# Optimization experiments

Measured on AMD Instinct MI355X. Metric: run time of the kernel, lower is better.

The kernel has to match this reference:

```python
import jax, jax.numpy as jnp
import numpy as np

N = 50000          # nodes
E = 800000         # edges
IN_C = 128
HID = 64
NUM_GRAPHS = 256
OUT_C = 8


def setup_inputs() -> dict:
    key = jax.random.key(0)
    k1, k2, k3, k4, k5, k6, k7 = jax.random.split(key, 7)
    x = jax.random.normal(k1, (N, IN_C), dtype=jnp.float32)
    edge_index = jax.random.randint(k2, (2, E), 0, N, dtype=jnp.int64)
    batch = jnp.sort(jax.random.randint(k3, (N,), 0, NUM_GRAPHS, dtype=jnp.int64))
    # GCNConv params (lin: in->hid, glorot-ish) and fc params (hid->8)
    W = jax.random.normal(k4, (IN_C, HID), dtype=jnp.float32) / np.sqrt(IN_C)
    b = jnp.zeros((HID,), dtype=jnp.float32)
    Wfc = jax.random.normal(k5, (HID, OUT_C), dtype=jnp.float32) / np.sqrt(HID)
    bfc = jnp.zeros((OUT_C,), dtype=jnp.float32)
    return {"x": x, "edge_index": edge_index, "batch": batch,
            "W": W, "b": b, "Wfc": Wfc, "bfc": bfc}


def reference(x, edge_index, batch, W, b, Wfc, bfc):
    n = x.shape[0]
    # GCNConv: linear transform first, then normalized propagation w/ self-loops
    x_lin = x @ W                                             # [N, HID]
    self_loops = jnp.arange(n, dtype=edge_index.dtype)
    row = jnp.concatenate([edge_index[0], self_loops])        # src
    col = jnp.concatenate([edge_index[1], self_loops])        # dst
    # symmetric normalization: deg over destinations (weight = 1)
    deg = jax.ops.segment_sum(jnp.ones_like(col, dtype=x.dtype), col,
                              num_segments=n)                 # [N]
    dinv = jnp.where(deg > 0, jax.lax.rsqrt(deg), 0.0)
    norm = dinv[row] * dinv[col]                              # [E+N]
    msg = x_lin[row] * norm[:, None]                          # gather + scale
    h = jax.ops.segment_sum(msg, col, num_segments=n) + b     # scatter-add
    h = jax.nn.relu(h)
    # global_mean_pool over batch ids
    sums = jax.ops.segment_sum(h, batch, num_segments=NUM_GRAPHS)
    cnts = jax.ops.segment_sum(jnp.ones((n,), dtype=x.dtype), batch,
                               num_segments=NUM_GRAPHS)
    pooled = sums / jnp.maximum(cnts, 1.0)[:, None]           # [G, HID]
    return pooled @ Wfc + bfc                                 # [G, 8]
```

## Files before the change

### kernel.cpp

```cpp
#include <hip/hip_runtime.h>
#include <stdint.h>

#define N_NODES 50000
#define N_EDGES 800000
#define IN_C    128
#define HID     64
#define NUM_G   256
#define OUT_C   8

#define NBH   64
#define ES    (N_EDGES / NBH)
#define NBIN  50048
#define NPK   (NBIN / 2)

#define NQ_H   4
#define BINS_H (NBIN / NQ_H)
#define PK_H   (BINS_H / 2)
#define NQ_S   8
#define BINS_S (NBIN / NQ_S)

#define NBLK_CSR 98

__device__ __forceinline__ void gload_lds16(const void* g, void* l) {
    __builtin_amdgcn_global_load_lds(
        (const __attribute__((address_space(1))) unsigned int*)g,
        (__attribute__((address_space(3))) unsigned int*)l, 16, 0, 0);
}

__device__ __forceinline__ unsigned short f2bf(float f) {
    union { float f; unsigned u; } v; v.f = f;
    unsigned r = v.u + 0x7fff + ((v.u >> 16) & 1);
    return (unsigned short)(r >> 16);
}

__device__ __forceinline__ float4 bf4(uint2 u) {
    union { unsigned u; float f; } a, b, c, d;
    a.u = u.x << 16;
    b.u = u.x & 0xffff0000u;
    c.u = u.y << 16;
    d.u = u.y & 0xffff0000u;
    return make_float4(a.f, b.f, c.f, d.f);
}

__global__ __launch_bounds__(256) void k_histB(const int* __restrict__ col,
                                               int* __restrict__ part,
                                               int* __restrict__ doneCnt) {
    __shared__ int lh[PK_H];
    const int tid = threadIdx.x;
    if (blockIdx.x == 0 && tid == 0)
        __hip_atomic_store(doneCnt, 0, __ATOMIC_RELAXED, __HIP_MEMORY_SCOPE_AGENT);
    const int r = blockIdx.x >> 2;
    const int q = blockIdx.x & 3;
    const int q0 = q * BINS_H;
    for (int i = tid; i < PK_H; i += 256) lh[i] = 0;
    __syncthreads();
    const int4* col4 = (const int4*)(col + r * ES);
#pragma unroll 2
    for (int j4 = tid; j4 < ES / 4; j4 += 256) {
        int4 c = col4[j4];
        unsigned d0 = (unsigned)(c.x - q0), d1 = (unsigned)(c.y - q0);
        unsigned d2 = (unsigned)(c.z - q0), d3 = (unsigned)(c.w - q0);
        if (d0 < BINS_H) atomicAdd(&lh[d0 >> 1], 1 << ((d0 & 1) * 16));
        if (d1 < BINS_H) atomicAdd(&lh[d1 >> 1], 1 << ((d1 & 1) * 16));
        if (d2 < BINS_H) atomicAdd(&lh[d2 >> 1], 1 << ((d2 & 1) * 16));
        if (d3 < BINS_H) atomicAdd(&lh[d3 >> 1], 1 << ((d3 & 1) * 16));
    }
    __syncthreads();
    int* dst = part + r * NPK + q * PK_H;
    for (int i = tid; i < PK_H; i += 256) dst[i] = lh[i];
}

__global__ __launch_bounds__(256) void k_csr(int* __restrict__ part,
                                             float* __restrict__ dinv,
                                             int* __restrict__ nstart,
                                             const int* __restrict__ batch,
                                             int* __restrict__ gstart,
                                             float* __restrict__ pooled,
                                             int* __restrict__ agg,
                                             int* __restrict__ doneCnt) {
    __shared__ int sScan[256];
    __shared__ int sAgg[NBLK_CSR];
    __shared__ int sPrefix;
    const int tid = threadIdx.x;
    const int b   = blockIdx.x;
    const int t   = b * 256 + tid;
    const bool valid = t < NPK;

    int s0 = 0, s1 = 0;
    if (valid) {
        int idx = t;
#pragma unroll 4
        for (int r = 0; r < NBH; ++r, idx += NPK) {
            int v = part[idx];
            part[idx] = s0 | (s1 << 16);
            s0 += v & 0xffff;
            s1 += (v >> 16) & 0xffff;
        }
        ((float2*)dinv)[t] = make_float2(rsqrtf((float)(s0 + 1)),
                                         rsqrtf((float)(s1 + 1)));
    }

    int ps = s0 + s1;
    sScan[tid] = ps;
    __syncthreads();
    int acc = ps;
#pragma unroll
    for (int off = 1; off < 256; off <<= 1) {
        int tv = (tid >= off) ? sScan[tid - off] : 0;
        __syncthreads();
        acc += tv;
        sScan[tid] = acc;
        __syncthreads();
    }
    const int excl  = acc - ps;
    const int total = sScan[255];

    if (tid == 0) {
        __hip_atomic_store(&agg[b], total, __ATOMIC_RELAXED, __HIP_MEMORY_SCOPE_AGENT);
        __hip_atomic_fetch_add(doneCnt, 1, __ATOMIC_RELEASE, __HIP_MEMORY_SCOPE_AGENT);
        while (__hip_atomic_load(doneCnt, __ATOMIC_ACQUIRE, __HIP_MEMORY_SCOPE_AGENT) < NBLK_CSR)
            __builtin_amdgcn_s_sleep(1);
    }
    __syncthreads();
    if (tid < NBLK_CSR)
        sAgg[tid] = __hip_atomic_load(&agg[tid], __ATOMIC_RELAXED, __HIP_MEMORY_SCOPE_AGENT);
    __syncthreads();
    if (tid == 0) {
        int p = 0;
        for (int j = 0; j < b; ++j) p += sAgg[j];
        sPrefix = p;
    }
    __syncthreads();

    if (valid) {
        int base = sPrefix + excl;
        ((int2*)nstart)[t] = make_int2(base, base + s0);
    }
    if (t <= NUM_G) {
        int lo = 0, hi = N_NODES;
        while (lo < hi) {
            int mid = (lo + hi) >> 1;
            if (batch[mid] < t) lo = mid + 1; else hi = mid;
        }
        gstart[t] = lo;
    }
    if (t < NUM_G * HID) pooled[t] = 0.f;
}

__global__ __launch_bounds__(256) void k_scat2(const int* __restrict__ row,
                                               const int* __restrict__ col,
                                               const int* __restrict__ part,
                                               const int* __restrict__ nstart,
                                               int* __restrict__ ed) {
    __shared__ int lc[BINS_S];
    const int tid = threadIdx.x;
    const int r = blockIdx.x >> 3;
    const int q = blockIdx.x & 7;
    const int q0 = q * BINS_S;
    for (int i = tid; i < BINS_S; i += 256) {
        int bin = q0 + i;
        int bb = part[r * NPK + (bin >> 1)];
        int off = (i & 1) ? ((bb >> 16) & 0xffff) : (bb & 0xffff);
        lc[i] = nstart[bin] + off;
    }
    __syncthreads();
    const int4* col4 = (const int4*)(col + r * ES);
    const int4* row4 = (const int4*)(row + r * ES);
#pragma unroll 2
    for (int j4 = tid; j4 < ES / 4; j4 += 256) {
        int4 c = col4[j4];
        int4 s = row4[j4];
        unsigned d0 = (unsigned)(c.x - q0), d1 = (unsigned)(c.y - q0);
        unsigned d2 = (unsigned)(c.z - q0), d3 = (unsigned)(c.w - q0);
        if (d0 < BINS_S) ed[atomicAdd(&lc[d0], 1)] = s.x;
        if (d1 < BINS_S) ed[atomicAdd(&lc[d1], 1)] = s.y;
        if (d2 < BINS_S) ed[atomicAdd(&lc[d2], 1)] = s.z;
        if (d3 < BINS_S) ed[atomicAdd(&lc[d3], 1)] = s.w;
    }
}

__global__ __launch_bounds__(256) void k_lin(const float* __restrict__ x,
                                             const float* __restrict__ W,
                                             const float* __restrict__ dinv,
                                             unsigned short* __restrict__ yb) {
    __shared__ float xs[64 * IN_C];
    __shared__ float Ws[IN_C * HID];
    const int tid = threadIdx.x;
    const size_t row0 = (size_t)blockIdx.x * 64;
    const int ln = tid & 63, wv = tid >> 6;

    {
        const char* wsrc = (const char*)W;
#pragma unroll
        for (int it = 0; it < 8; ++it) {
            int c = wv * 8 + it;
            gload_lds16(wsrc + c * 1024 + ln * 16, (char*)Ws + c * 1024);
        }
    }
    if (row0 + 64 <= N_NODES) {
        const char* gsrc = (const char*)(x + row0 * IN_C);
#pragma unroll
        for (int it = 0; it < 8; ++it) {
            int c = wv * 8 + it;
            gload_lds16(gsrc + c * 1024 + ln * 16, (char*)xs + c * 1024);
        }
    } else {
        const float4* src = (const float4*)(x + row0 * IN_C);
        for (int i4 = tid; i4 < 2048; i4 += 256) {
            int r = i4 >> 5;
            float4 v = make_float4(0.f, 0.f, 0.f, 0.f);
            if (row0 + r < N_NODES) v = src[i4];
            ((float4*)xs)[i4] = v;
        }
    }
    __syncthreads();

    const int ty = tid >> 4, tx = tid & 15;
    const int r0 = ty * 4, c0 = tx * 4;
    float acc[4][4] = {};

#define AC(ai, kk) ((kk)==0 ? av##ai.x : (kk)==1 ? av##ai.y : (kk)==2 ? av##ai.z : av##ai.w)
#define ROWF(ai, kk, bv) \
    acc[ai][0] = fmaf(AC(ai,kk), bv.x, acc[ai][0]); \
    acc[ai][1] = fmaf(AC(ai,kk), bv.y, acc[ai][1]); \
    acc[ai][2] = fmaf(AC(ai,kk), bv.z, acc[ai][2]); \
    acc[ai][3] = fmaf(AC(ai,kk), bv.w, acc[ai][3]);
#define K4(kk, bv) ROWF(0,kk,bv) ROWF(1,kk,bv) ROWF(2,kk,bv) ROWF(3,kk,bv)

    for (int k = 0; k < IN_C; k += 4) {
        float4 av0 = *(const float4*)&xs[(r0+0)*IN_C + k];
        float4 av1 = *(const float4*)&xs[(r0+1)*IN_C + k];
        float4 av2 = *(const float4*)&xs[(r0+2)*IN_C + k];
        float4 av3 = *(const float4*)&xs[(r0+3)*IN_C + k];
        float4 bv0 = *(const float4*)&Ws[(k+0)*HID + c0];
        float4 bv1 = *(const float4*)&Ws[(k+1)*HID + c0];
        float4 bv2 = *(const float4*)&Ws[(k+2)*HID + c0];
        float4 bv3 = *(const float4*)&Ws[(k+3)*HID + c0];
        K4(0, bv0) K4(1, bv1) K4(2, bv2) K4(3, bv3)
    }
#undef K4
#undef ROWF
#undef AC

#pragma unroll
    for (int i = 0; i < 4; ++i) {
        size_t r = row0 + r0 + i;
        if (r < N_NODES) {
            float dv = dinv[r];
            ushort4 o;
            o.x = f2bf(acc[i][0] * dv);
            o.y = f2bf(acc[i][1] * dv);
            o.z = f2bf(acc[i][2] * dv);
            o.w = f2bf(acc[i][3] * dv);
            *(ushort4*)&yb[r * HID + c0] = o;
        }
    }
}

#define NPT 8
__global__ __launch_bounds__(256) void k_gpool(const int* __restrict__ ed,
                                               const int* __restrict__ nstart,
                                               const float* __restrict__ dinv,
                                               const unsigned short* __restrict__ yb,
                                               const int* __restrict__ batch,
                                               const float* __restrict__ bias,
                                               float* __restrict__ pooled) {
    const int lane = threadIdx.x & 63;
    const int grp  = lane >> 4;
    const int sl   = lane & 15;
    const int node0 = (blockIdx.x * 4 + (threadIdx.x >> 6)) * NPT;
    if (node0 >= N_NODES) return;
    const float4 b4 = *(const float4*)&bias[4 * sl];
    float4 pacc = make_float4(0.f, 0.f, 0.f, 0.f);
    int    cur  = -1;
#pragma unroll 1
    for (int t0 = 0; t0 < NPT; ++t0) {
        int node = node0 + t0;
        if (node >= N_NODES) break;
        const int n0 = nstart[node], n1 = nstart[node + 1];
        float4 facc = make_float4(0.f, 0.f, 0.f, 0.f);
        int t = n0 + grp;
        const int nfull8 = n0 + ((n1 - n0) & ~7);
#pragma unroll 1
        for (; t < nfull8; t += 8) {
            int srcA = ed[t];
            int srcB = ed[t + 4];
            uint2 ua = *(const uint2*)&yb[(size_t)srcA * HID + 4 * sl];
            uint2 ub = *(const uint2*)&yb[(size_t)srcB * HID + 4 * sl];
            float4 va = bf4(ua), vb = bf4(ub);
            facc.x += va.x + vb.x;
            facc.y += va.y + vb.y;
            facc.z += va.z + vb.z;
            facc.w += va.w + vb.w;
        }
#pragma unroll
        for (int step = 0; step < 2; ++step) {
            bool act = t < n1;
            int tt = act ? t : 0;
            int src = ed[tt];
            uint2 u = *(const uint2*)&yb[(size_t)src * HID + 4 * sl];
            if (act) {
                float4 v = bf4(u);
                facc.x += v.x; facc.y += v.y; facc.z += v.z; facc.w += v.w;
            }
            t += 4;
        }
        facc.x += __shfl_xor(facc.x, 16, 64);
        facc.y += __shfl_xor(facc.y, 16, 64);
        facc.z += __shfl_xor(facc.z, 16, 64);
        facc.w += __shfl_xor(facc.w, 16, 64);
        facc.x += __shfl_xor(facc.x, 32, 64);
        facc.y += __shfl_xor(facc.y, 32, 64);
        facc.z += __shfl_xor(facc.z, 32, 64);
        facc.w += __shfl_xor(facc.w, 32, 64);
        uint2 us = *(const uint2*)&yb[(size_t)node * HID + 4 * sl];
        float4 vs = bf4(us);
        float dv = dinv[node];
        float4 hv;
        hv.x = fmaxf((facc.x + vs.x) * dv + b4.x, 0.f);
        hv.y = fmaxf((facc.y + vs.y) * dv + b4.y, 0.f);
        hv.z = fmaxf((facc.z + vs.z) * dv + b4.z, 0.f);
        hv.w = fmaxf((facc.w + vs.w) * dv + b4.w, 0.f);
        int bg = batch[node];
        if (bg != cur) {
            if (cur >= 0 && grp == 0) {
                atomicAdd(&pooled[cur * HID + 4 * sl + 0], pacc.x);
                atomicAdd(&pooled[cur * HID + 4 * sl + 1], pacc.y);
                atomicAdd(&pooled[cur * HID + 4 * sl + 2], pacc.z);
                atomicAdd(&pooled[cur * HID + 4 * sl + 3], pacc.w);
            }
            cur  = bg;
            pacc = hv;
        } else {
            pacc.x += hv.x; pacc.y += hv.y; pacc.z += hv.z; pacc.w += hv.w;
        }
    }
    if (cur >= 0 && grp == 0) {
        atomicAdd(&pooled[cur * HID + 4 * sl + 0], pacc.x);
        atomicAdd(&pooled[cur * HID + 4 * sl + 1], pacc.y);
        atomicAdd(&pooled[cur * HID + 4 * sl + 2], pacc.z);
        atomicAdd(&pooled[cur * HID + 4 * sl + 3], pacc.w);
    }
}

__global__ void k_out(const float* __restrict__ pooled, const int* __restrict__ gstart,
                      const float* __restrict__ Wfc, const float* __restrict__ bfc,
                      float* __restrict__ out) {
    int idx = blockIdx.x * blockDim.x + threadIdx.x;
    int g = idx >> 3;
    int o = idx & 7;
    float inv = 1.f / fmaxf((float)(gstart[g + 1] - gstart[g]), 1.f);
    float acc = 0.f;
#pragma unroll
    for (int k = 0; k < HID; ++k) acc += pooled[g * HID + k] * Wfc[k * OUT_C + o];
    out[idx] = acc * inv + bfc[o];
}

extern "C" void kernel_launch(void* const* d_in, const int* in_sizes, int n_in,
                              void* d_out, int out_size, void* d_ws, size_t ws_size,
                              hipStream_t stream) {
    const float* x     = (const float*)d_in[0];
    const int*   eidx  = (const int*)d_in[1];
    const int*   batch = (const int*)d_in[2];
    const float* W     = (const float*)d_in[3];
    const float* b     = (const float*)d_in[4];
    const float* Wfc   = (const float*)d_in[5];
    const float* bfc   = (const float*)d_in[6];
    float*       out   = (float*)d_out;

    const int* row = eidx;
    const int* col = eidx + N_EDGES;

    char* p = (char*)d_ws;
    int*            part = (int*)p;
    unsigned short* yb   = (unsigned short*)p;
    p += (size_t)NBH * NPK * 4;
    float* dinv   = (float*)p;  p += (size_t)NBIN * 4;
    float* pooled = (float*)p;  p += (size_t)NUM_G * HID * 4;
    int*   nstart = (int*)p;    p += (size_t)(NBIN + 4) * 4;
    int*   gstart = (int*)p;    p += 1040;
    int*   agg    = (int*)p;    p += 400;
    int*   doneCnt= (int*)p;    p += 16;
    int*   ed     = (int*)p;

    k_histB <<<NBH * NQ_H, 256, 0, stream>>>(col, part, doneCnt);
    k_csr   <<<NBLK_CSR, 256, 0, stream>>>(part, dinv, nstart, batch, gstart, pooled, agg, doneCnt);
    k_scat2 <<<NBH * NQ_S, 256, 0, stream>>>(row, col, part, nstart, ed);
    k_lin   <<<(N_NODES + 63) / 64, 256, 0, stream>>>(x, W, dinv, yb);
    k_gpool <<<(N_NODES + 4 * NPT - 1) / (4 * NPT), 256, 0, stream>>>(ed, nstart, dinv, yb, batch, b, pooled);
    k_out   <<<8, 256, 0, stream>>>(pooled, gstart, Wfc, bfc, out);
}
```

Baseline: 102.3 us.

## Fuse CSR build and linear transform into one persistent kernel with packed edges

Merges histogram, scan, and scatter into one kernel using grid-wide spin barriers, and runs the x@W GEMM concurrently in extra blocks of the same launch. Edges are packed as a 16-bit source id plus an fp16 precomputed norm, which removes the dinv scaling from the GEMM epilogue. The final FC layer runs in the last-finishing gpool block instead of a separate launch. This cuts the launch count from six to three and overlaps the GEMM with graph construction. In exchange it depends on all build blocks being co-resident for the spin barriers, and adds fp16 rounding of the norms.

```diff
diff --git a/kernel.cpp b/kernel.cpp
--- a/kernel.cpp
+++ b/kernel.cpp
@@ -1,4 +1,5 @@
 #include <hip/hip_runtime.h>
+#include <hip/hip_fp16.h>
 #include <stdint.h>
 
 #define N_NODES 50000
@@ -16,344 +17,345 @@
 #define NQ_H   4
 #define BINS_H (NBIN / NQ_H)
 #define PK_H   (BINS_H / 2)
-#define NQ_S   8
+#define NQ_S   4
 #define BINS_S (NBIN / NQ_S)
 
-#define NBLK_CSR 98
-
-__device__ __forceinline__ void gload_lds16(const void* g, void* l) {
-    __builtin_amdgcn_global_load_lds(
-        (const __attribute__((address_space(1))) unsigned int*)g,
-        (__attribute__((address_space(3))) unsigned int*)l, 16, 0, 0);
-}
+#define NBLK_CSR   98
+#define NBLK_BUILD 256
+#define NBLK_LIN   512
+#define NTILE      1563
+#define GPOOL_GRID 1563
 
 __device__ __forceinline__ unsigned short f2bf(float f) {
     union { float f; unsigned u; } v; v.f = f;
     unsigned r = v.u + 0x7fff + ((v.u >> 16) & 1);
     return (unsigned short)(r >> 16);
 }
-
 __device__ __forceinline__ float4 bf4(uint2 u) {
     union { unsigned u; float f; } a, b, c, d;
-    a.u = u.x << 16;
-    b.u = u.x & 0xffff0000u;
-    c.u = u.y << 16;
-    d.u = u.y & 0xffff0000u;
+    a.u = u.x << 16;  b.u = u.x & 0xffff0000u;
+    c.u = u.y << 16;  d.u = u.y & 0xffff0000u;
     return make_float4(a.f, b.f, c.f, d.f);
 }
-
-__global__ __launch_bounds__(256) void k_histB(const int* __restrict__ col,
-                                               int* __restrict__ part,
-                                               int* __restrict__ doneCnt) {
-    __shared__ int lh[PK_H];
-    const int tid = threadIdx.x;
-    if (blockIdx.x == 0 && tid == 0)
-        __hip_atomic_store(doneCnt, 0, __ATOMIC_RELAXED, __HIP_MEMORY_SCOPE_AGENT);
-    const int r = blockIdx.x >> 2;
-    const int q = blockIdx.x & 3;
-    const int q0 = q * BINS_H;
-    for (int i = tid; i < PK_H; i += 256) lh[i] = 0;
-    __syncthreads();
-    const int4* col4 = (const int4*)(col + r * ES);
-#pragma unroll 2
-    for (int j4 = tid; j4 < ES / 4; j4 += 256) {
-        int4 c = col4[j4];
-        unsigned d0 = (unsigned)(c.x - q0), d1 = (unsigned)(c.y - q0);
-        unsigned d2 = (unsigned)(c.z - q0), d3 = (unsigned)(c.w - q0);
-        if (d0 < BINS_H) atomicAdd(&lh[d0 >> 1], 1 << ((d0 & 1) * 16));
-        if (d1 < BINS_H) atomicAdd(&lh[d1 >> 1], 1 << ((d1 & 1) * 16));
-        if (d2 < BINS_H) atomicAdd(&lh[d2 >> 1], 1 << ((d2 & 1) * 16));
-        if (d3 < BINS_H) atomicAdd(&lh[d3 >> 1], 1 << ((d3 & 1) * 16));
-    }
-    __syncthreads();
-    int* dst = part + r * NPK + q * PK_H;
-    for (int i = tid; i < PK_H; i += 256) dst[i] = lh[i];
-}
-
-__global__ __launch_bounds__(256) void k_csr(int* __restrict__ part,
-                                             float* __restrict__ dinv,
-                                             int* __restrict__ nstart,
-                                             const int* __restrict__ batch,
-                                             int* __restrict__ gstart,
-                                             float* __restrict__ pooled,
-                                             int* __restrict__ agg,
-                                             int* __restrict__ doneCnt) {
-    __shared__ int sScan[256];
-    __shared__ int sAgg[NBLK_CSR];
-    __shared__ int sPrefix;
+__device__ __forceinline__ float h2f(unsigned hu) {
+    union { __half h; unsigned short u; } c; c.u = (unsigned short)hu;
+    return __half2float(c.h);
+}
+
+__global__ void k_z(float* __restrict__ pooled, int* __restrict__ cnt) {
+    int i = blockIdx.x * 256 + threadIdx.x;
+    pooled[i] = 0.f;
+    if (i < 8) cnt[i] = 0;
+}
+
+__global__ __launch_bounds__(256, 3) void k_build(
+        const int* __restrict__ row, const int* __restrict__ col,
+        const int* __restrict__ batch,
+        const float* __restrict__ x, const float* __restrict__ W,
+        int* __restrict__ part, float* __restrict__ dinv,
+        int* __restrict__ nstart, int* __restrict__ gstart,
+        unsigned* __restrict__ ed, unsigned short* __restrict__ yb,
+        int* __restrict__ agg, int* __restrict__ cnt) {
+    __shared__ int smemI[12512];
     const int tid = threadIdx.x;
     const int b   = blockIdx.x;
-    const int t   = b * 256 + tid;
-    const bool valid = t < NPK;
-
-    int s0 = 0, s1 = 0;
-    if (valid) {
-        int idx = t;
+
+    if (b >= NBLK_BUILD) {
+        float* xs = (float*)smemI;
+        float* Ws = (float*)smemI + 4224;
+        {
+            const float4* wsrc = (const float4*)W;
+            float4*       wdst = (float4*)Ws;
+#pragma unroll
+            for (int j = 0; j < 8; ++j) wdst[tid + 256 * j] = wsrc[tid + 256 * j];
+        }
+        const int ty = tid >> 4, tx = tid & 15;
+        const int r0 = ty * 2, c0 = tx * 4;
+        for (int tile = b - NBLK_BUILD; tile < NTILE; tile += NBLK_LIN) {
+            const int row0 = tile * 32;
+            __syncthreads();
+            {
+                const float4* src = (const float4*)(x + (size_t)row0 * IN_C);
+                for (int i4 = tid; i4 < 1024; i4 += 256) {
+                    int r = i4 >> 5, c4 = i4 & 31;
+                    float4 v = make_float4(0.f, 0.f, 0.f, 0.f);
+                    if (row0 + r < N_NODES) v = src[i4];
+                    *(float4*)&xs[r * 132 + c4 * 4] = v;
+                }
+            }
+            __syncthreads();
+            float acc[2][4] = {};
+#define FMA4(a_, bv_, r_) { acc[r_][0]=fmaf(a_,bv_.x,acc[r_][0]); acc[r_][1]=fmaf(a_,bv_.y,acc[r_][1]); \
+                            acc[r_][2]=fmaf(a_,bv_.z,acc[r_][2]); acc[r_][3]=fmaf(a_,bv_.w,acc[r_][3]); }
+            for (int k = 0; k < IN_C; k += 4) {
+                float4 a0 = *(float4*)&xs[(r0 + 0) * 132 + k];
+                float4 a1 = *(float4*)&xs[(r0 + 1) * 132 + k];
+                float4 b0 = *(const float4*)&Ws[(k + 0) * HID + c0];
+                float4 b1 = *(const float4*)&Ws[(k + 1) * HID + c0];
+                float4 b2 = *(const float4*)&Ws[(k + 2) * HID + c0];
+                float4 b3 = *(const float4*)&Ws[(k + 3) * HID + c0];
+                FMA4(a0.x, b0, 0) FMA4(a0.y, b1, 0) FMA4(a0.z, b2, 0) FMA4(a0.w, b3, 0)
+                FMA4(a1.x, b0, 1) FMA4(a1.y, b1, 1) FMA4(a1.z, b2, 1) FMA4(a1.w, b3, 1)
+            }
+#undef FMA4
+#pragma unroll
+            for (int i = 0; i < 2; ++i) {
+                int r = row0 + r0 + i;
+                if (r < N_NODES) {
+                    ushort4 o;
+                    o.x = f2bf(acc[i][0]); o.y = f2bf(acc[i][1]);
+                    o.z = f2bf(acc[i][2]); o.w = f2bf(acc[i][3]);
+                    *(ushort4*)&yb[(size_t)r * HID + c0] = o;
+                }
+            }
+        }
+        return;
+    }
+
+    {
+        int* lh = smemI;
+        const int rr = b >> 2, q = b & 3, q0 = q * BINS_H;
+        for (int i = tid; i < PK_H; i += 256) lh[i] = 0;
+        __syncthreads();
+        const int4* col4 = (const int4*)(col + rr * ES);
+        for (int j4 = tid; j4 < ES / 4; j4 += 256) {
+            int4 c = col4[j4];
+            unsigned d0 = (unsigned)(c.x - q0), d1 = (unsigned)(c.y - q0);
+            unsigned d2 = (unsigned)(c.z - q0), d3 = (unsigned)(c.w - q0);
+            if (d0 < BINS_H) atomicAdd(&lh[d0 >> 1], 1 << ((d0 & 1) * 16));
+            if (d1 < BINS_H) atomicAdd(&lh[d1 >> 1], 1 << ((d1 & 1) * 16));
+            if (d2 < BINS_H) atomicAdd(&lh[d2 >> 1], 1 << ((d2 & 1) * 16));
+            if (d3 < BINS_H) atomicAdd(&lh[d3 >> 1], 1 << ((d3 & 1) * 16));
+        }
+        __syncthreads();
+        int* dst = part + rr * NPK + q * PK_H;
+        for (int i = tid; i < PK_H; i += 256) dst[i] = lh[i];
+        __syncthreads();
+    }
+    if (tid == 0) {
+        __hip_atomic_fetch_add(&cnt[0], 1, __ATOMIC_RELEASE, __HIP_MEMORY_SCOPE_AGENT);
+        while (__hip_atomic_load(&cnt[0], __ATOMIC_ACQUIRE, __HIP_MEMORY_SCOPE_AGENT) < NBLK_BUILD)
+            __builtin_amdgcn_s_sleep(2);
+    }
+    __syncthreads();
+
+    if (b < NBLK_CSR) {
+        int* sScan   = smemI;
+        int* sAgg    = smemI + 256;
+        int* sPrefix = smemI + 256 + 128;
+        const int t = b * 256 + tid;
+        const bool valid = t < NPK;
+        int s0 = 0, s1 = 0;
+        if (valid) {
+            int idx = t;
 #pragma unroll 4
-        for (int r = 0; r < NBH; ++r, idx += NPK) {
-            int v = part[idx];
-            part[idx] = s0 | (s1 << 16);
-            s0 += v & 0xffff;
-            s1 += (v >> 16) & 0xffff;
-        }
-        ((float2*)dinv)[t] = make_float2(rsqrtf((float)(s0 + 1)),
-                                         rsqrtf((float)(s1 + 1)));
-    }
-
-    int ps = s0 + s1;
-    sScan[tid] = ps;
+            for (int r = 0; r < NBH; ++r, idx += NPK) {
+                int v = part[idx];
+                part[idx] = s0 | (s1 << 16);
+                s0 += v & 0xffff;
+                s1 += (v >> 16) & 0xffff;
+            }
+            ((float2*)dinv)[t] = make_float2(rsqrtf((float)(s0 + 1)),
+                                             rsqrtf((float)(s1 + 1)));
+        }
+        int ps = s0 + s1;
+        sScan[tid] = ps;
+        __syncthreads();
+        int acc = ps;
+#pragma unroll
+        for (int off = 1; off < 256; off <<= 1) {
+            int tv = (tid >= off) ? sScan[tid - off] : 0;
+            __syncthreads();
+            acc += tv;
+            sScan[tid] = acc;
+            __syncthreads();
+        }
+        const int excl  = acc - ps;
+        const int total = sScan[255];
+        if (tid == 0) {
+            __hip_atomic_store(&agg[b], total, __ATOMIC_RELAXED, __HIP_MEMORY_SCOPE_AGENT);
+            __hip_atomic_fetch_add(&cnt[1], 1, __ATOMIC_RELEASE, __HIP_MEMORY_SCOPE_AGENT);
+            while (__hip_atomic_load(&cnt[1], __ATOMIC_ACQUIRE, __HIP_MEMORY_SCOPE_AGENT) < NBLK_CSR)
+                __builtin_amdgcn_s_sleep(2);
+        }
+        __syncthreads();
+        if (tid < NBLK_CSR)
+            sAgg[tid] = __hip_atomic_load(&agg[tid], __ATOMIC_RELAXED, __HIP_MEMORY_SCOPE_AGENT);
+        __syncthreads();
+        if (tid == 0) {
+            int p = 0;
+            for (int j = 0; j < b; ++j) p += sAgg[j];
+            sPrefix[0] = p;
+        }
+        __syncthreads();
+        if (valid) {
+            int base = sPrefix[0] + excl;
+            ((int2*)nstart)[t] = make_int2(base, base + s0);
+        }
+        if (t <= NUM_G) {
+            int lo = 0, hi = N_NODES;
+            while (lo < hi) {
+                int mid = (lo + hi) >> 1;
+                if (batch[mid] < t) lo = mid + 1; else hi = mid;
+            }
+            gstart[t] = lo;
+        }
+        __syncthreads();
+        if (tid == 0)
+            __hip_atomic_fetch_add(&cnt[2], 1, __ATOMIC_RELEASE, __HIP_MEMORY_SCOPE_AGENT);
+    }
+    if (tid == 0) {
+        while (__hip_atomic_load(&cnt[2], __ATOMIC_ACQUIRE, __HIP_MEMORY_SCOPE_AGENT) < NBLK_CSR)
+            __builtin_amdgcn_s_sleep(2);
+    }
     __syncthreads();
-    int acc = ps;
-#pragma unroll
-    for (int off = 1; off < 256; off <<= 1) {
-        int tv = (tid >= off) ? sScan[tid - off] : 0;
-        __syncthreads();
-        acc += tv;
-        sScan[tid] = acc;
-        __syncthreads();
-    }
-    const int excl  = acc - ps;
-    const int total = sScan[255];
-
-    if (tid == 0) {
-        __hip_atomic_store(&agg[b], total, __ATOMIC_RELAXED, __HIP_MEMORY_SCOPE_AGENT);
-        __hip_atomic_fetch_add(doneCnt, 1, __ATOMIC_RELEASE, __HIP_MEMORY_SCOPE_AGENT);
-        while (__hip_atomic_load(doneCnt, __ATOMIC_ACQUIRE, __HIP_MEMORY_SCOPE_AGENT) < NBLK_CSR)
-            __builtin_amdgcn_s_sleep(1);
-    }
-    __syncthreads();
-    if (tid < NBLK_CSR)
-        sAgg[tid] = __hip_atomic_load(&agg[tid], __ATOMIC_RELAXED, __HIP_MEMORY_SCOPE_AGENT);
-    __syncthreads();
-    if (tid == 0) {
-        int p = 0;
-        for (int j = 0; j < b; ++j) p += sAgg[j];
-        sPrefix = p;
-    }
-    __syncthreads();
-
-    if (valid) {
-        int base = sPrefix + excl;
-        ((int2*)nstart)[t] = make_int2(base, base + s0);
-    }
-    if (t <= NUM_G) {
-        int lo = 0, hi = N_NODES;
-        while (lo < hi) {
-            int mid = (lo + hi) >> 1;
-            if (batch[mid] < t) lo = mid + 1; else hi = mid;
-        }
-        gstart[t] = lo;
-    }
-    if (t < NUM_G * HID) pooled[t] = 0.f;
-}
-
-__global__ __launch_bounds__(256) void k_scat2(const int* __restrict__ row,
-                                               const int* __restrict__ col,
-                                               const int* __restrict__ part,
-                                               const int* __restrict__ nstart,
-                                               int* __restrict__ ed) {
-    __shared__ int lc[BINS_S];
-    const int tid = threadIdx.x;
-    const int r = blockIdx.x >> 3;
-    const int q = blockIdx.x & 7;
-    const int q0 = q * BINS_S;
-    for (int i = tid; i < BINS_S; i += 256) {
-        int bin = q0 + i;
-        int bb = part[r * NPK + (bin >> 1)];
-        int off = (i & 1) ? ((bb >> 16) & 0xffff) : (bb & 0xffff);
-        lc[i] = nstart[bin] + off;
-    }
-    __syncthreads();
-    const int4* col4 = (const int4*)(col + r * ES);
-    const int4* row4 = (const int4*)(row + r * ES);
-#pragma unroll 2
-    for (int j4 = tid; j4 < ES / 4; j4 += 256) {
-        int4 c = col4[j4];
-        int4 s = row4[j4];
-        unsigned d0 = (unsigned)(c.x - q0), d1 = (unsigned)(c.y - q0);
-        unsigned d2 = (unsigned)(c.z - q0), d3 = (unsigned)(c.w - q0);
-        if (d0 < BINS_S) ed[atomicAdd(&lc[d0], 1)] = s.x;
-        if (d1 < BINS_S) ed[atomicAdd(&lc[d1], 1)] = s.y;
-        if (d2 < BINS_S) ed[atomicAdd(&lc[d2], 1)] = s.z;
-        if (d3 < BINS_S) ed[atomicAdd(&lc[d3], 1)] = s.w;
-    }
-}
-
-__global__ __launch_bounds__(256) void k_lin(const float* __restrict__ x,
-                                             const float* __restrict__ W,
-                                             const float* __restrict__ dinv,
-                                             unsigned short* __restrict__ yb) {
-    __shared__ float xs[64 * IN_C];
-    __shared__ float Ws[IN_C * HID];
-    const int tid = threadIdx.x;
-    const size_t row0 = (size_t)blockIdx.x * 64;
-    const int ln = tid & 63, wv = tid >> 6;
 
     {
-        const char* wsrc = (const char*)W;
-#pragma unroll
-        for (int it = 0; it < 8; ++it) {
-            int c = wv * 8 + it;
-            gload_lds16(wsrc + c * 1024 + ln * 16, (char*)Ws + c * 1024);
-        }
-    }
-    if (row0 + 64 <= N_NODES) {
-        const char* gsrc = (const char*)(x + row0 * IN_C);
-#pragma unroll
-        for (int it = 0; it < 8; ++it) {
-            int c = wv * 8 + it;
-            gload_lds16(gsrc + c * 1024 + ln * 16, (char*)xs + c * 1024);
-        }
-    } else {
-        const float4* src = (const float4*)(x + row0 * IN_C);
-        for (int i4 = tid; i4 < 2048; i4 += 256) {
-            int r = i4 >> 5;
-            float4 v = make_float4(0.f, 0.f, 0.f, 0.f);
-            if (row0 + r < N_NODES) v = src[i4];
-            ((float4*)xs)[i4] = v;
-        }
-    }
-    __syncthreads();
-
-    const int ty = tid >> 4, tx = tid & 15;
-    const int r0 = ty * 4, c0 = tx * 4;
-    float acc[4][4] = {};
-
-#define AC(ai, kk) ((kk)==0 ? av##ai.x : (kk)==1 ? av##ai.y : (kk)==2 ? av##ai.z : av##ai.w)
-#define ROWF(ai, kk, bv) \
-    acc[ai][0] = fmaf(AC(ai,kk), bv.x, acc[ai][0]); \
-    acc[ai][1] = fmaf(AC(ai,kk), bv.y, acc[ai][1]); \
-    acc[ai][2] = fmaf(AC(ai,kk), bv.z, acc[ai][2]); \
-    acc[ai][3] = fmaf(AC(ai,kk), bv.w, acc[ai][3]);
-#define K4(kk, bv) ROWF(0,kk,bv) ROWF(1,kk,bv) ROWF(2,kk,bv) ROWF(3,kk,bv)
-
-    for (int k = 0; k < IN_C; k += 4) {
-        float4 av0 = *(const float4*)&xs[(r0+0)*IN_C + k];
-        float4 av1 = *(const float4*)&xs[(r0+1)*IN_C + k];
-        float4 av2 = *(const float4*)&xs[(r0+2)*IN_C + k];
-        float4 av3 = *(const float4*)&xs[(r0+3)*IN_C + k];
-        float4 bv0 = *(const float4*)&Ws[(k+0)*HID + c0];
-        float4 bv1 = *(const float4*)&Ws[(k+1)*HID + c0];
-        float4 bv2 = *(const float4*)&Ws[(k+2)*HID + c0];
-        float4 bv3 = *(const float4*)&Ws[(k+3)*HID + c0];
-        K4(0, bv0) K4(1, bv1) K4(2, bv2) K4(3, bv3)
-    }
-#undef K4
-#undef ROWF
-#undef AC
-
-#pragma unroll
-    for (int i = 0; i < 4; ++i) {
-        size_t r = row0 + r0 + i;
-        if (r < N_NODES) {
-            float dv = dinv[r];
-            ushort4 o;
-            o.x = f2bf(acc[i][0] * dv);
-            o.y = f2bf(acc[i][1] * dv);
-            o.z = f2bf(acc[i][2] * dv);
-            o.w = f2bf(acc[i][3] * dv);
-            *(ushort4*)&yb[r * HID + c0] = o;
-        }
+        int* lc = smemI;
+        const int rr = b >> 2, q = b & 3, q0 = q * BINS_S;
+        for (int i = tid; i < BINS_S; i += 256) {
+            int bin = q0 + i;
+            int bb  = part[rr * NPK + (bin >> 1)];
+            int off = (i & 1) ? ((bb >> 16) & 0xffff) : (bb & 0xffff);
+            lc[i] = nstart[bin] + off;
+        }
+        __syncthreads();
+        const int4* col4 = (const int4*)(col + rr * ES);
+        const int4* row4 = (const int4*)(row + rr * ES);
+#define PROC(dv_, sv_) { unsigned dd = (unsigned)((dv_) - q0); \
+        if (dd < BINS_S) { int pos = atomicAdd(&lc[dd], 1); \
+            float nrm = dinv[sv_] * dinv[dv_]; \
+            union { __half h; unsigned short u; } cv; cv.h = __float2half(nrm); \
+            ed[pos] = (unsigned)(sv_) | ((unsigned)cv.u << 16); } }
+        for (int j4 = tid; j4 < ES / 4; j4 += 256) {
+            int4 c = col4[j4];
+            int4 s = row4[j4];
+            PROC(c.x, s.x) PROC(c.y, s.y) PROC(c.z, s.z) PROC(c.w, s.w)
+        }
+#undef PROC
     }
 }
 
 #define NPT 8
-__global__ __launch_bounds__(256) void k_gpool(const int* __restrict__ ed,
+__global__ __launch_bounds__(256) void k_gpool(const unsigned* __restrict__ ed,
                                                const int* __restrict__ nstart,
                                                const float* __restrict__ dinv,
                                                const unsigned short* __restrict__ yb,
                                                const int* __restrict__ batch,
                                                const float* __restrict__ bias,
-                                               float* __restrict__ pooled) {
-    const int lane = threadIdx.x & 63;
+                                               float* __restrict__ pooled,
+                                               const int* __restrict__ gstart,
+                                               const float* __restrict__ Wfc,
+                                               const float* __restrict__ bfc,
+                                               float* __restrict__ out,
+                                               int* __restrict__ cnt) {
+    const int tid  = threadIdx.x;
+    const int lane = tid & 63;
     const int grp  = lane >> 4;
     const int sl   = lane & 15;
-    const int node0 = (blockIdx.x * 4 + (threadIdx.x >> 6)) * NPT;
-    if (node0 >= N_NODES) return;
-    const float4 b4 = *(const float4*)&bias[4 * sl];
-    float4 pacc = make_float4(0.f, 0.f, 0.f, 0.f);
-    int    cur  = -1;
+    const int node0 = (blockIdx.x * 4 + (tid >> 6)) * NPT;
+    if (node0 < N_NODES) {
+        const float4 b4 = *(const float4*)&bias[4 * sl];
+        float4 pacc = make_float4(0.f, 0.f, 0.f, 0.f);
+        int    cur  = -1;
 #pragma unroll 1
-    for (int t0 = 0; t0 < NPT; ++t0) {
-        int node = node0 + t0;
-        if (node >= N_NODES) break;
-        const int n0 = nstart[node], n1 = nstart[node + 1];
-        float4 facc = make_float4(0.f, 0.f, 0.f, 0.f);
-        int t = n0 + grp;
-        const int nfull8 = n0 + ((n1 - n0) & ~7);
+        for (int t0 = 0; t0 < NPT; ++t0) {
+            int node = node0 + t0;
+            if (node >= N_NODES) break;
+            const int n0 = nstart[node], n1 = nstart[node + 1];
+            float4 facc = make_float4(0.f, 0.f, 0.f, 0.f);
+            int t = n0 + grp;
+            const int nfull8 = n0 + ((n1 - n0) & ~7);
 #pragma unroll 1
-        for (; t < nfull8; t += 8) {
-            int srcA = ed[t];
-            int srcB = ed[t + 4];
-            uint2 ua = *(const uint2*)&yb[(size_t)srcA * HID + 4 * sl];
-            uint2 ub = *(const uint2*)&yb[(size_t)srcB * HID + 4 * sl];
-            float4 va = bf4(ua), vb = bf4(ub);
-            facc.x += va.x + vb.x;
-            facc.y += va.y + vb.y;
-            facc.z += va.z + vb.z;
-            facc.w += va.w + vb.w;
-        }
-#pragma unroll
-        for (int step = 0; step < 2; ++step) {
-            bool act = t < n1;
-            int tt = act ? t : 0;
-            int src = ed[tt];
-            uint2 u = *(const uint2*)&yb[(size_t)src * HID + 4 * sl];
-            if (act) {
-                float4 v = bf4(u);
-                facc.x += v.x; facc.y += v.y; facc.z += v.z; facc.w += v.w;
-            }
-            t += 4;
-        }
-        facc.x += __shfl_xor(facc.x, 16, 64);
-        facc.y += __shfl_xor(facc.y, 16, 64);
-        facc.z += __shfl_xor(facc.z, 16, 64);
-        facc.w += __shfl_xor(facc.w, 16, 64);
-        facc.x += __shfl_xor(facc.x, 32, 64);
-        facc.y += __shfl_xor(facc.y, 32, 64);
-        facc.z += __shfl_xor(facc.z, 32, 64);
-        facc.w += __shfl_xor(facc.w, 32, 64);
-        uint2 us = *(const uint2*)&yb[(size_t)node * HID + 4 * sl];
-        float4 vs = bf4(us);
-        float dv = dinv[node];
-        float4 hv;
-        hv.x = fmaxf((facc.x + vs.x) * dv + b4.x, 0.f);
-        hv.y = fmaxf((facc.y + vs.y) * dv + b4.y, 0.f);
-        hv.z = fmaxf((facc.z + vs.z) * dv + b4.z, 0.f);
-        hv.w = fmaxf((facc.w + vs.w) * dv + b4.w, 0.f);
-        int bg = batch[node];
-        if (bg != cur) {
-            if (cur >= 0 && grp == 0) {
-                atomicAdd(&pooled[cur * HID + 4 * sl + 0], pacc.x);
-                atomicAdd(&pooled[cur * HID + 4 * sl + 1], pacc.y);
-                atomicAdd(&pooled[cur * HID + 4 * sl + 2], pacc.z);
-                atomicAdd(&pooled[cur * HID + 4 * sl + 3], pacc.w);
-            }
-            cur  = bg;
-            pacc = hv;
-        } else {
-            pacc.x += hv.x; pacc.y += hv.y; pacc.z += hv.z; pacc.w += hv.w;
-        }
-    }
-    if (cur >= 0 && grp == 0) {
-        atomicAdd(&pooled[cur * HID + 4 * sl + 0], pacc.x);
-        atomicAdd(&pooled[cur * HID + 4 * sl + 1], pacc.y);
-        atomicAdd(&pooled[cur * HID + 4 * sl + 2], pacc.z);
-        atomicAdd(&pooled[cur * HID + 4 * sl + 3], pacc.w);
-    }
-}
-
-__global__ void k_out(const float* __restrict__ pooled, const int* __restrict__ gstart,
-                      const float* __restrict__ Wfc, const float* __restrict__ bfc,
-                      float* __restrict__ out) {
-    int idx = blockIdx.x * blockDim.x + threadIdx.x;
-    int g = idx >> 3;
-    int o = idx & 7;
-    float inv = 1.f / fmaxf((float)(gstart[g + 1] - gstart[g]), 1.f);
-    float acc = 0.f;
-#pragma unroll
-    for (int k = 0; k < HID; ++k) acc += pooled[g * HID + k] * Wfc[k * OUT_C + o];
-    out[idx] = acc * inv + bfc[o];
+            for (; t < nfull8; t += 8) {
+                unsigned uA = ed[t];
+                unsigned uB = ed[t + 4];
+                int sA = uA & 0xffffu, sB = uB & 0xffffu;
+                float nA = h2f(uA >> 16), nB = h2f(uB >> 16);
+                uint2 ua = *(const uint2*)&yb[(size_t)sA * HID + 4 * sl];
+                uint2 ub = *(const uint2*)&yb[(size_t)sB * HID + 4 * sl];
+                float4 va = bf4(ua), vb = bf4(ub);
+                facc.x = fmaf(nA, va.x, fmaf(nB, vb.x, facc.x));
+                facc.y = fmaf(nA, va.y, fmaf(nB, vb.y, facc.y));
+                facc.z = fmaf(nA, va.z, fmaf(nB, vb.z, facc.z));
+                facc.w = fmaf(nA, va.w, fmaf(nB, vb.w, facc.w));
+            }
+#pragma unroll
+            for (int step = 0; step < 2; ++step) {
+                bool act = t < n1;
+                unsigned u = ed[act ? t : 0];
+                int src = u & 0xffffu;
+                uint2 uy = *(const uint2*)&yb[(size_t)src * HID + 4 * sl];
+                if (act) {
+                    float nm = h2f(u >> 16);
+                    float4 v = bf4(uy);
+                    facc.x = fmaf(nm, v.x, facc.x);
+                    facc.y = fmaf(nm, v.y, facc.y);
+                    facc.z = fmaf(nm, v.z, facc.z);
+                    facc.w = fmaf(nm, v.w, facc.w);
+                }
+                t += 4;
+            }
+            facc.x += __shfl_xor(facc.x, 16, 64);
+            facc.y += __shfl_xor(facc.y, 16, 64);
+            facc.z += __shfl_xor(facc.z, 16, 64);
+            facc.w += __shfl_xor(facc.w, 16, 64);
+            facc.x += __shfl_xor(facc.x, 32, 64);
+            facc.y += __shfl_xor(facc.y, 32, 64);
+            facc.z += __shfl_xor(facc.z, 32, 64);
+            facc.w += __shfl_xor(facc.w, 32, 64);
+            uint2 us = *(const uint2*)&yb[(size_t)node * HID + 4 * sl];
+            float4 vs = bf4(us);
+            float dv = dinv[node];
+            float sw = dv * dv;
+            float4 hv;
+            hv.x = fmaxf(fmaf(vs.x, sw, facc.x) + b4.x, 0.f);
+            hv.y = fmaxf(fmaf(vs.y, sw, facc.y) + b4.y, 0.f);
+            hv.z = fmaxf(fmaf(vs.z, sw, facc.z) + b4.z, 0.f);
+            hv.w = fmaxf(fmaf(vs.w, sw, facc.w) + b4.w, 0.f);
+            int bg = batch[node];
+            if (bg != cur) {
+                if (cur >= 0 && grp == 0) {
+                    atomicAdd(&pooled[cur * HID + 4 * sl + 0], pacc.x);
+                    atomicAdd(&pooled[cur * HID + 4 * sl + 1], pacc.y);
+                    atomicAdd(&pooled[cur * HID + 4 * sl + 2], pacc.z);
+                    atomicAdd(&pooled[cur * HID + 4 * sl + 3], pacc.w);
+                }
+                cur  = bg;
+                pacc = hv;
+            } else {
+                pacc.x += hv.x; pacc.y += hv.y; pacc.z += hv.z; pacc.w += hv.w;
+            }
+        }
+        if (cur >= 0 && grp == 0) {
+            atomicAdd(&pooled[cur * HID + 4 * sl + 0], pacc.x);
+            atomicAdd(&pooled[cur * HID + 4 * sl + 1], pacc.y);
+            atomicAdd(&pooled[cur * HID + 4 * sl + 2], pacc.z);
+            atomicAdd(&pooled[cur * HID + 4 * sl + 3], pacc.w);
+        }
+    }
+    __shared__ int lastFlag;
+    __syncthreads();
+    if (tid == 0) {
+        int prev = __hip_atomic_fetch_add(&cnt[3], 1, __ATOMIC_ACQ_REL, __HIP_MEMORY_SCOPE_AGENT);
+        lastFlag = (prev == GPOOL_GRID - 1) ? 1 : 0;
+    }
+    __syncthreads();
+    if (lastFlag) {
+        int g = tid;
+        int g0 = gstart[g], g1 = gstart[g + 1];
+        float inv = 1.f / fmaxf((float)(g1 - g0), 1.f);
+        float acc[OUT_C] = {};
+        for (int k = 0; k < HID; ++k) {
+            float pv = pooled[g * HID + k];
+#pragma unroll
+            for (int o = 0; o < OUT_C; ++o)
+                acc[o] = fmaf(pv, Wfc[k * OUT_C + o], acc[o]);
+        }
+#pragma unroll
+        for (int o = 0; o < OUT_C; ++o)
+            out[g * OUT_C + o] = acc[o] * inv + bfc[o];
+    }
 }
 
 extern "C" void kernel_launch(void* const* d_in, const int* in_sizes, int n_in,
@@ -372,21 +374,20 @@
     const int* col = eidx + N_EDGES;
 
     char* p = (char*)d_ws;
-    int*            part = (int*)p;
-    unsigned short* yb   = (unsigned short*)p;
-    p += (size_t)NBH * NPK * 4;
+    unsigned short* yb = (unsigned short*)p;  p += (size_t)N_NODES * HID * 2;
+    int*   part   = (int*)p;    p += (size_t)NBH * NPK * 4;
     float* dinv   = (float*)p;  p += (size_t)NBIN * 4;
     float* pooled = (float*)p;  p += (size_t)NUM_G * HID * 4;
-    int*   nstart = (int*)p;    p += (size_t)(NBIN + 4) * 4;
+    int*   nstart = (int*)p;    p += (size_t)(NBIN + 8) * 4;
     int*   gstart = (int*)p;    p += 1040;
-    int*   agg    = (int*)p;    p += 400;
-    int*   doneCnt= (int*)p;    p += 16;
-    int*   ed     = (int*)p;
-
-    k_histB <<<NBH * NQ_H, 256, 0, stream>>>(col, part, doneCnt);
-    k_csr   <<<NBLK_CSR, 256, 0, stream>>>(part, dinv, nstart, batch, gstart, pooled, agg, doneCnt);
-    k_scat2 <<<NBH * NQ_S, 256, 0, stream>>>(row, col, part, nstart, ed);
-    k_lin   <<<(N_NODES + 63) / 64, 256, 0, stream>>>(x, W, dinv, yb);
-    k_gpool <<<(N_NODES + 4 * NPT - 1) / (4 * NPT), 256, 0, stream>>>(ed, nstart, dinv, yb, batch, b, pooled);
-    k_out   <<<8, 256, 0, stream>>>(pooled, gstart, Wfc, bfc, out);
-}
+    int*   agg    = (int*)p;    p += 512;
+    int*   cnt    = (int*)p;    p += 64;
+    unsigned* ed  = (unsigned*)p;
+
+    k_z     <<<64, 256, 0, stream>>>(pooled, cnt);
+    k_build <<<NBLK_BUILD + NBLK_LIN, 256, 0, stream>>>(row, col, batch, x, W,
+                                                        part, dinv, nstart, gstart,
+                                                        ed, yb, agg, cnt);
+    k_gpool <<<GPOOL_GRID, 256, 0, stream>>>(ed, nstart, dinv, yb, batch, b,
+                                             pooled, gstart, Wfc, bfc, out, cnt);
+}
```

Result: slower. 203.4 us (+98.9%).
